# Performance work log

Hardware: AMD Instinct MI355X
Metric: run time of the kernel (lower is better)

The kernel has to match this reference:

```python
import jax, jax.numpy as jnp
import numpy as np

E = 1024      # embed_dim (== embed_dim_)
NH = 8        # num_heads
HD = E // NH  # head_dim
BS1 = 2048
BS2 = 2048
EPS = 1e-5


def _layernorm(x, g, b):
    m = jnp.mean(x, axis=-1, keepdims=True)
    v = jnp.mean(jnp.square(x - m), axis=-1, keepdims=True)
    return (x - m) * jax.lax.rsqrt(v + EPS) * g + b


def setup_inputs() -> dict:
    key = jax.random.key(0)
    ks = jax.random.split(key, 16)
    s = 1.0 / np.sqrt(E)
    s4 = 1.0 / np.sqrt(4 * E)
    inp = {
        "x1": jax.random.normal(ks[0], (BS1, E), jnp.float32),
        "x2": jax.random.normal(ks[1], (BS2, E), jnp.float32),
        "Wq": jax.random.uniform(ks[2], (E, E), jnp.float32, -s, s),
        "bq": jax.random.uniform(ks[3], (E,), jnp.float32, -s, s),
        "Wk": jax.random.uniform(ks[4], (E, E), jnp.float32, -s, s),
        "bk": jax.random.uniform(ks[5], (E,), jnp.float32, -s, s),
        "Wv": jax.random.uniform(ks[6], (E, E), jnp.float32, -s, s),
        "bv": jax.random.uniform(ks[7], (E,), jnp.float32, -s, s),
        "Wo": jax.random.uniform(ks[8], (E, E), jnp.float32, -s, s),
        "bo": jax.random.uniform(ks[9], (E,), jnp.float32, -s, s),
        "W1": jax.random.uniform(ks[10], (4 * E, E), jnp.float32, -s, s),
        "b1": jax.random.uniform(ks[11], (4 * E,), jnp.float32, -s, s),
        "W2": jax.random.uniform(ks[12], (E, 4 * E), jnp.float32, -s4, s4),
        "b2": jax.random.uniform(ks[13], (E,), jnp.float32, -s4, s4),
        "g1": jnp.ones((E,), jnp.float32),
        "be1": jnp.zeros((E,), jnp.float32),
        "g2": jnp.ones((E,), jnp.float32),
        "be2": jnp.zeros((E,), jnp.float32),
    }
    return inp


def reference(x1, x2, Wq, bq, Wk, bk, Wv, bv, Wo, bo, W1, b1, W2, b2, g1, be1, g2, be2):
    scale = HD ** -0.5
    # Projections; attention runs over the batch axis (n=bs1, m=bs2)
    q = (x1 @ Wq.T + bq).reshape(BS1, NH, HD)   # [n,h,d]
    k = (x2 @ Wk.T + bk).reshape(BS2, NH, HD)   # [m,h,d]
    v = (x2 @ Wv.T + bv).reshape(BS2, NH, HD)   # [m,h,d]
    scores = jnp.einsum('nhd,mhd->nmh', q, k) * scale  # [n,m,h]
    # NOTE: faithful to source: softmax over the HEADS axis (dim=-1)
    probs = jax.nn.softmax(scores, axis=-1)
    # dropout is identity in eval mode
    attn = jnp.einsum('nmh,mhd->nhd', probs, v).reshape(BS1, E)
    attn = attn @ Wo.T + bo
    h = _layernorm(x1 + attn, g1, be1)
    ffn = jax.nn.relu(h @ W1.T + b1) @ W2.T + b2
    return _layernorm(h + ffn, g2, be2)
```

## Files before the change

kernel.cpp:

```cpp
#include <hip/hip_runtime.h>

#define BS 2048
#define EMB 1024
#define NHEAD 8
#define HDIM 128

typedef unsigned short u16;
typedef __attribute__((ext_vector_type(8))) short bf16x8;
typedef __attribute__((ext_vector_type(4))) float f32x4;

__device__ __forceinline__ u16 f32_bf16(float f) {
  unsigned u = __float_as_uint(f);
  u += 0x7fffu + ((u >> 16) & 1u);
  return (u16)(u >> 16);
}
__device__ __forceinline__ float bf2f(u16 x) {
  return __uint_as_float((unsigned)x << 16);
}

__device__ __forceinline__ void gld_lds16(const void* g, void* l) {
  __builtin_amdgcn_global_load_lds(
      (const __attribute__((address_space(1))) void*)g,
      (__attribute__((address_space(3))) void*)l, 16, 0, 0);
}

struct CvtArgs { const float* src[8]; };
__global__ __launch_bounds__(256) void cvt_all(CvtArgs a, u16* __restrict__ dst) {
  long i = (long)blockIdx.x * 256 + threadIdx.x;
  int seg = (int)(i >> 18);
  const float* src; long b;
  if (seg < 2)       { src = a.src[0]; b = 0; }
  else if (seg < 4)  { src = a.src[1]; b = 2L << 18; }
  else if (seg == 4) { src = a.src[2]; b = 4L << 18; }
  else if (seg == 5) { src = a.src[3]; b = 5L << 18; }
  else if (seg == 6) { src = a.src[4]; b = 6L << 18; }
  else if (seg == 7) { src = a.src[5]; b = 7L << 18; }
  else if (seg < 12) { src = a.src[6]; b = 8L << 18; }
  else               { src = a.src[7]; b = 12L << 18; }
  float4 v = ((const float4*)src)[i - b];
  ushort4 o;
  o.x = f32_bf16(v.x); o.y = f32_bf16(v.y); o.z = f32_bf16(v.z); o.w = f32_bf16(v.w);
  ((ushort4*)dst)[i] = o;
}

__device__ __forceinline__ void gemm_core(
    const u16* __restrict__ A, const u16* __restrict__ B, void* __restrict__ Cp,
    const float* __restrict__ bias, int K, int lda, int ldb, int ldc,
    long cbase, int mode, int relu, int m0, int n0) {
  __shared__ __align__(16) u16 As[128 * 32];
  __shared__ __align__(16) u16 Bs[128 * 32];
  const int t = threadIdx.x;
  const int lane = t & 63, l15 = lane & 15, quad = lane >> 4;
  const int wv = t >> 6, wr = wv & 1, wc = wv >> 1;
  const int wbase = t & ~63;

  f32x4 acc[4][4];
#pragma unroll
  for (int r = 0; r < 4; ++r)
#pragma unroll
    for (int c = 0; c < 4; ++c) acc[r][c] = (f32x4){0.f, 0.f, 0.f, 0.f};

  for (int k0 = 0; k0 < K; k0 += 32) {
#pragma unroll
    for (int i = 0; i < 2; ++i) {
      int s = i * 256 + t;
      gld_lds16(A + (long)(m0 + (s >> 2)) * lda + k0 + (s & 3) * 8,
                As + (i * 256 + wbase) * 8);
    }
#pragma unroll
    for (int i = 0; i < 2; ++i) {
      int s = i * 256 + t;
      gld_lds16(B + (long)(n0 + (s >> 2)) * ldb + k0 + (s & 3) * 8,
                Bs + (i * 256 + wbase) * 8);
    }
    __syncthreads();
    bf16x8 fa[4], fb[4];
#pragma unroll
    for (int r = 0; r < 4; ++r)
      fa[r] = *(const bf16x8*)&As[(wr * 64 + r * 16 + l15) * 32 + quad * 8];
#pragma unroll
    for (int c = 0; c < 4; ++c)
      fb[c] = *(const bf16x8*)&Bs[(wc * 64 + c * 16 + l15) * 32 + quad * 8];
#pragma unroll
    for (int r = 0; r < 4; ++r)
#pragma unroll
      for (int c = 0; c < 4; ++c)
        acc[r][c] = __builtin_amdgcn_mfma_f32_16x16x32_bf16(fa[r], fb[c], acc[r][c], 0, 0, 0);
    __syncthreads();
  }

#pragma unroll
  for (int r = 0; r < 4; ++r)
#pragma unroll
    for (int c = 0; c < 4; ++c) {
      const int m = m0 + wr * 64 + r * 16 + quad * 4;
      const int n = n0 + wc * 64 + c * 16 + l15;
      const float bv = bias ? bias[n] : 0.f;
      f32x4 v = acc[r][c];
      if (mode == 2) {
        ushort4 o;
        o.x = f32_bf16(v[0] + bv);
        o.y = f32_bf16(v[1] + bv);
        o.z = f32_bf16(v[2] + bv);
        o.w = f32_bf16(v[3] + bv);
        *(ushort4*)((u16*)Cp + cbase + (long)n * ldc + m) = o;
      } else {
#pragma unroll
        for (int i = 0; i < 4; ++i) {
          float x = v[i] + bv;
          if (relu) x = fmaxf(x, 0.f);
          if (mode == 0)
            ((float*)Cp)[cbase + (long)(m + i) * ldc + n] = x;
          else
            ((u16*)Cp)[cbase + (long)(m + i) * ldc + n] = f32_bf16(x);
        }
      }
    }
}

__global__ __launch_bounds__(256) void gemm_bt_k(
    const u16* __restrict__ A, const u16* __restrict__ B, void* __restrict__ C,
    const float* __restrict__ bias, int K, int lda, int ldb, int ldc,
    long aOffZ, long bOffZ, long cOffZ, int mode, int relu) {
  gemm_core(A + (long)blockIdx.z * aOffZ, B + (long)blockIdx.z * bOffZ, C, bias,
            K, lda, ldb, ldc, (long)blockIdx.z * cOffZ, mode, relu,
            blockIdx.y * 128, blockIdx.x * 128);
}

__global__ __launch_bounds__(256) void qkv_kernel(
    const u16* __restrict__ x1b, const u16* __restrict__ x2b,
    const u16* __restrict__ Wqb, const u16* __restrict__ Wkb, const u16* __restrict__ Wvb,
    const float* __restrict__ bq, const float* __restrict__ bk, const float* __restrict__ bv,
    u16* __restrict__ Qb, u16* __restrict__ Kb, u16* __restrict__ Vt) {
  const int z = blockIdx.z;
  const u16* A = (z == 0) ? x1b : x2b;
  const u16* B = (z == 0) ? Wqb : (z == 1) ? Wkb : Wvb;
  void* C = (z == 0) ? (void*)Qb : (z == 1) ? (void*)Kb : (void*)Vt;
  const float* bias = (z == 0) ? bq : (z == 1) ? bk : bv;
  const int mode = (z == 2) ? 2 : 1;
  const int ldc = (z == 2) ? 2048 : 1024;
  gemm_core(A, B, C, bias, 1024, 1024, 1024, ldc, 0, mode, 0,
            blockIdx.y * 128, blockIdx.x * 128);
}

__global__ __launch_bounds__(1024, 4) void attn_fused(
    const u16* __restrict__ Q, const u16* __restrict__ Km, const u16* __restrict__ Vt,
    u16* __restrict__ p0, u16* __restrict__ p1, u16* __restrict__ p2, u16* __restrict__ p3) {
  __shared__ __align__(16) u16 Qs[32 * 1024];
  __shared__ __align__(16) u16 Ps[8 * 32 * 128];
  const int t = threadIdx.x;
  const int lane = t & 63, l15 = lane & 15, quad = lane >> 4;
  const int w = t >> 6, wbase = t & ~63;
  const int mw = w & 7, nh = w >> 3;
  const int n0 = blockIdx.x * 32;
  const int mz = blockIdx.y * 512;
  u16* part = (blockIdx.y == 0) ? p0 : (blockIdx.y == 1) ? p1 : (blockIdx.y == 2) ? p2 : p3;

#pragma unroll
  for (int i = 0; i < 4; ++i) {
    int s = i * 1024 + t;
    int n = s >> 7;
    int kel = (((s & 127) << 3) ^ ((n & 7) << 3));
    gld_lds16(Q + (long)(n0 + n) * 1024 + kel, Qs + (i * 1024 + wbase) * 8);
  }

  const int nq = nh * 16 + l15;
  const int swz3 = (nq & 7) << 3;
  const int swz4 = (nq & 7) << 4;

  f32x4 accp[8];
#pragma unroll
  for (int c = 0; c < 8; ++c) accp[c] = (f32x4){0.f, 0.f, 0.f, 0.f};

  for (int it = 0; it < 4; ++it) {
    __syncthreads();
    f32x4 accs[8];
#pragma unroll
    for (int h = 0; h < 8; ++h) accs[h] = (f32x4){0.f, 0.f, 0.f, 0.f};
    const u16* krow = Km + (long)(mz + it * 128 + mw * 16 + l15) * 1024;
#pragma unroll
    for (int h = 0; h < 8; ++h)
#pragma unroll
      for (int kk = 0; kk < 4; ++kk) {
        bf16x8 kf = *(const bf16x8*)&krow[h * 128 + kk * 32 + quad * 8];
        bf16x8 qf = *(const bf16x8*)&Qs[nq * 1024 + ((h * 128 + kk * 32 + quad * 8) ^ swz3)];
        accs[h] = __builtin_amdgcn_mfma_f32_16x16x32_bf16(kf, qf, accs[h], 0, 0, 0);
      }
    const float scale = 0.08838834764831845f;
#pragma unroll
    for (int i = 0; i < 4; ++i) {
      float mx = accs[0][i];
#pragma unroll
      for (int h = 1; h < 8; ++h) mx = fmaxf(mx, accs[h][i]);
      float sum = 0.f;
#pragma unroll
      for (int h = 0; h < 8; ++h) {
        float e = __expf((accs[h][i] - mx) * scale);
        accs[h][i] = e;
        sum += e;
      }
      float inv = 1.f / sum;
#pragma unroll
      for (int h = 0; h < 8; ++h) accs[h][i] *= inv;
    }
#pragma unroll
    for (int h = 0; h < 8; ++h) {
      ushort4 o;
      o.x = f32_bf16(accs[h][0]);
      o.y = f32_bf16(accs[h][1]);
      o.z = f32_bf16(accs[h][2]);
      o.w = f32_bf16(accs[h][3]);
      *(ushort4*)((char*)Ps + h * 8192 + nq * 256 + ((mw * 32 + quad * 8) ^ swz4)) = o;
    }
    __syncthreads();
#pragma unroll
    for (int mq = 0; mq < 4; ++mq) {
      bf16x8 pa = *(const bf16x8*)((const char*)Ps + mw * 8192 + nq * 256 +
                                   ((mq * 64 + quad * 16) ^ swz4));
      const u16* vb = Vt + (long)(mw * 128) * 2048 + mz + it * 128 + mq * 32 + quad * 8;
#pragma unroll
      for (int c = 0; c < 8; ++c) {
        bf16x8 vf = *(const bf16x8*)&vb[(long)(c * 16 + l15) * 2048];
        accp[c] = __builtin_amdgcn_mfma_f32_16x16x32_bf16(pa, vf, accp[c], 0, 0, 0);
      }
    }
  }
#pragma unroll
  for (int c = 0; c < 8; ++c)
#pragma unroll
    for (int i = 0; i < 4; ++i)
      part[(long)(n0 + nh * 16 + quad * 4 + i) * 1024 + mw * 128 + c * 16 + l15] =
          f32_bf16(accp[c][i]);
}

__global__ __launch_bounds__(256) void reduce4p_bf16(
    const u16* __restrict__ p0, const u16* __restrict__ p1,
    const u16* __restrict__ p2, const u16* __restrict__ p3, u16* __restrict__ out) {
  long i = (long)blockIdx.x * 256 + threadIdx.x;
  ushort4 a = ((const ushort4*)p0)[i];
  ushort4 b = ((const ushort4*)p1)[i];
  ushort4 c = ((const ushort4*)p2)[i];
  ushort4 d = ((const ushort4*)p3)[i];
  ushort4 o;
  o.x = f32_bf16(bf2f(a.x) + bf2f(b.x) + bf2f(c.x) + bf2f(d.x));
  o.y = f32_bf16(bf2f(a.y) + bf2f(b.y) + bf2f(c.y) + bf2f(d.y));
  o.z = f32_bf16(bf2f(a.z) + bf2f(b.z) + bf2f(c.z) + bf2f(d.z));
  o.w = f32_bf16(bf2f(a.w) + bf2f(b.w) + bf2f(c.w) + bf2f(d.w));
  ((ushort4*)out)[i] = o;
}

__global__ __launch_bounds__(256) void ln_residual_p4(
    const float* __restrict__ x,
    const u16* __restrict__ p0, const u16* __restrict__ p1,
    const u16* __restrict__ p2, const u16* __restrict__ p3,
    const float* __restrict__ colb, const float* __restrict__ g, const float* __restrict__ b,
    float* __restrict__ out32, u16* __restrict__ out16) {
  const int row = blockIdx.x, t = threadIdx.x;
  const long base = (long)row * EMB;
  float4 v = ((const float4*)(x + base))[t];
  ushort4 a0 = ((const ushort4*)(p0 + base))[t];
  ushort4 a1 = ((const ushort4*)(p1 + base))[t];
  ushort4 a2 = ((const ushort4*)(p2 + base))[t];
  ushort4 a3 = ((const ushort4*)(p3 + base))[t];
  float4 cb = ((const float4*)colb)[t];
  v.x += bf2f(a0.x) + bf2f(a1.x) + bf2f(a2.x) + bf2f(a3.x) + cb.x;
  v.y += bf2f(a0.y) + bf2f(a1.y) + bf2f(a2.y) + bf2f(a3.y) + cb.y;
  v.z += bf2f(a0.z) + bf2f(a1.z) + bf2f(a2.z) + bf2f(a3.z) + cb.z;
  v.w += bf2f(a0.w) + bf2f(a1.w) + bf2f(a2.w) + bf2f(a3.w) + cb.w;
  float s = v.x + v.y + v.z + v.w;
  float q = v.x * v.x + v.y * v.y + v.z * v.z + v.w * v.w;
#pragma unroll
  for (int off = 32; off > 0; off >>= 1) {
    s += __shfl_xor(s, off);
    q += __shfl_xor(q, off);
  }
  __shared__ float red[8];
  const int wv = t >> 6, lane = t & 63;
  if (lane == 0) { red[wv] = s; red[4 + wv] = q; }
  __syncthreads();
  s = red[0] + red[1] + red[2] + red[3];
  q = red[4] + red[5] + red[6] + red[7];
  const float mean = s * (1.f / EMB);
  const float var = q * (1.f / EMB) - mean * mean;
  const float rstd = rsqrtf(var + 1e-5f);
  float4 gg = ((const float4*)g)[t];
  float4 bb = ((const float4*)b)[t];
  float4 o;
  o.x = (v.x - mean) * rstd * gg.x + bb.x;
  o.y = (v.y - mean) * rstd * gg.y + bb.y;
  o.z = (v.z - mean) * rstd * gg.z + bb.z;
  o.w = (v.w - mean) * rstd * gg.w + bb.w;
  ((float4*)(out32 + base))[t] = o;
  if (out16) {
    ushort4 ho;
    ho.x = f32_bf16(o.x); ho.y = f32_bf16(o.y); ho.z = f32_bf16(o.z); ho.w = f32_bf16(o.w);
    ((ushort4*)(out16 + base))[t] = ho;
  }
}

extern "C" void kernel_launch(void* const* d_in, const int* in_sizes, int n_in,
                              void* d_out, int out_size, void* d_ws, size_t ws_size,
                              hipStream_t stream) {
  const float* x1 = (const float*)d_in[0];
  const float* x2 = (const float*)d_in[1];
  const float* Wq = (const float*)d_in[2];
  const float* bq = (const float*)d_in[3];
  const float* Wk = (const float*)d_in[4];
  const float* bk = (const float*)d_in[5];
  const float* Wv = (const float*)d_in[6];
  const float* bv = (const float*)d_in[7];
  const float* Wo = (const float*)d_in[8];
  const float* bo = (const float*)d_in[9];
  const float* W1 = (const float*)d_in[10];
  const float* b1 = (const float*)d_in[11];
  const float* W2 = (const float*)d_in[12];
  const float* b2 = (const float*)d_in[13];
  const float* g1 = (const float*)d_in[14];
  const float* be1 = (const float*)d_in[15];
  const float* g2 = (const float*)d_in[16];
  const float* be2 = (const float*)d_in[17];

  char* ws = (char*)d_ws;
  const size_t MB = 1ull << 20;
  u16* x1b = (u16*)(ws + 0 * MB);
  u16* x2b = (u16*)(ws + 4 * MB);
  u16* Wqb = (u16*)(ws + 8 * MB);
  u16* Wkb = (u16*)(ws + 10 * MB);
  u16* Wvb = (u16*)(ws + 12 * MB);
  u16* Wob = (u16*)(ws + 14 * MB);
  u16* W1b = (u16*)(ws + 16 * MB);
  u16* W2b = (u16*)(ws + 24 * MB);
  u16* Qb  = (u16*)(ws + 32 * MB);
  u16* Kb  = (u16*)(ws + 36 * MB);
  u16* Vtb = (u16*)(ws + 40 * MB);
  u16* attnb = (u16*)(ws + 44 * MB);
  u16* aP[4] = {(u16*)(ws + 48 * MB), (u16*)(ws + 52 * MB),
                (u16*)(ws + 56 * MB), (u16*)(ws + 60 * MB)};
  u16* woP[4] = {(u16*)(ws + 48 * MB), (u16*)(ws + 52 * MB),
                 (u16*)(ws + 56 * MB), (u16*)(ws + 60 * MB)};
  float* h32  = (float*)(ws + 64 * MB);
  u16*  h16   = (u16*)(ws + 72 * MB);
  u16*  ffn1b = (u16*)(ws + 76 * MB);
  u16* f2P[4] = {(u16*)(ws + 92 * MB), (u16*)(ws + 96 * MB),
                 (u16*)(ws + 100 * MB), (u16*)(ws + 104 * MB)};

  CvtArgs ca;
  ca.src[0] = x1; ca.src[1] = x2; ca.src[2] = Wq; ca.src[3] = Wk;
  ca.src[4] = Wv; ca.src[5] = Wo; ca.src[6] = W1; ca.src[7] = W2;
  cvt_all<<<16384, 256, 0, stream>>>(ca, (u16*)ws);

  qkv_kernel<<<dim3(8, 16, 3), 256, 0, stream>>>(x1b, x2b, Wqb, Wkb, Wvb, bq, bk, bv, Qb, Kb, Vtb);

  attn_fused<<<dim3(64, 4), 1024, 0, stream>>>(Qb, Kb, Vtb, aP[0], aP[1], aP[2], aP[3]);

  reduce4p_bf16<<<2048, 256, 0, stream>>>(aP[0], aP[1], aP[2], aP[3], attnb);

  gemm_bt_k<<<dim3(8, 16, 4), 256, 0, stream>>>(attnb, Wob, woP[0], nullptr,
                                                256, 1024, 1024, 1024,
                                                256, 256, (long)BS * 1024, 1, 0);

  ln_residual_p4<<<2048, 256, 0, stream>>>(x1, woP[0], woP[1], woP[2], woP[3],
                                           bo, g1, be1, h32, h16);

  gemm_bt_k<<<dim3(32, 16, 1), 256, 0, stream>>>(h16, W1b, ffn1b, b1,
                                                 1024, 1024, 1024, 4096,
                                                 0, 0, 0, 1, 1);

  gemm_bt_k<<<dim3(8, 16, 4), 256, 0, stream>>>(ffn1b, W2b, f2P[0], nullptr,
                                                1024, 4096, 4096, 1024,
                                                1024, 1024, (long)BS * 1024, 1, 0);

  ln_residual_p4<<<2048, 256, 0, stream>>>(h32, f2P[0], f2P[1], f2P[2], f2P[3],
                                           b2, g2, be2, (float*)d_out, nullptr);
}
```

Baseline: 389.5 us.

## Shrink attention block to 16 query rows and read Q directly from global

The attention kernel now processes 16 query rows per block with 512 threads, not 32 rows with 1024 threads, and launches twice as many blocks. The Q tile is no longer staged into LDS; each wave loads Q fragments straight from global memory, and K/V fragment loads are batched ahead of the MFMA chains. This removes the large LDS allocation and the initial barrier so more blocks can be resident and loads can overlap. In exchange, K and V are re-read from global/L2 by twice as many blocks.

Measured after the change: 447.1 us. +14.8%, slower.

```diff
diff --git a/kernel.cpp b/kernel.cpp
--- a/kernel.cpp
+++ b/kernel.cpp
@@ -143,49 +143,43 @@
             blockIdx.y * 128, blockIdx.x * 128);
 }
 
-__global__ __launch_bounds__(1024, 4) void attn_fused(
+__global__ __launch_bounds__(512, 4) void attn_fused(
     const u16* __restrict__ Q, const u16* __restrict__ Km, const u16* __restrict__ Vt,
     u16* __restrict__ p0, u16* __restrict__ p1, u16* __restrict__ p2, u16* __restrict__ p3) {
-  __shared__ __align__(16) u16 Qs[32 * 1024];
-  __shared__ __align__(16) u16 Ps[8 * 32 * 128];
+  __shared__ __align__(16) u16 Ps[8 * 16 * 128];
   const int t = threadIdx.x;
   const int lane = t & 63, l15 = lane & 15, quad = lane >> 4;
-  const int w = t >> 6, wbase = t & ~63;
-  const int mw = w & 7, nh = w >> 3;
-  const int n0 = blockIdx.x * 32;
+  const int w = t >> 6;
+  const int n0 = blockIdx.x * 16;
   const int mz = blockIdx.y * 512;
   u16* part = (blockIdx.y == 0) ? p0 : (blockIdx.y == 1) ? p1 : (blockIdx.y == 2) ? p2 : p3;
 
-#pragma unroll
-  for (int i = 0; i < 4; ++i) {
-    int s = i * 1024 + t;
-    int n = s >> 7;
-    int kel = (((s & 127) << 3) ^ ((n & 7) << 3));
-    gld_lds16(Q + (long)(n0 + n) * 1024 + kel, Qs + (i * 1024 + wbase) * 8);
-  }
-
-  const int nq = nh * 16 + l15;
-  const int swz3 = (nq & 7) << 3;
-  const int swz4 = (nq & 7) << 4;
-
   f32x4 accp[8];
 #pragma unroll
   for (int c = 0; c < 8; ++c) accp[c] = (f32x4){0.f, 0.f, 0.f, 0.f};
 
+  const u16* qrow = Q + (long)(n0 + l15) * 1024 + quad * 8;
+
   for (int it = 0; it < 4; ++it) {
-    __syncthreads();
+    const int mb = mz + it * 128;
     f32x4 accs[8];
 #pragma unroll
     for (int h = 0; h < 8; ++h) accs[h] = (f32x4){0.f, 0.f, 0.f, 0.f};
-    const u16* krow = Km + (long)(mz + it * 128 + mw * 16 + l15) * 1024;
-#pragma unroll
-    for (int h = 0; h < 8; ++h)
+
+    const u16* krow = Km + (long)(mb + w * 16 + l15) * 1024 + quad * 8;
+#pragma unroll
+    for (int h = 0; h < 8; ++h) {
+      bf16x8 kf[4], qf[4];
 #pragma unroll
       for (int kk = 0; kk < 4; ++kk) {
-        bf16x8 kf = *(const bf16x8*)&krow[h * 128 + kk * 32 + quad * 8];
-        bf16x8 qf = *(const bf16x8*)&Qs[nq * 1024 + ((h * 128 + kk * 32 + quad * 8) ^ swz3)];
-        accs[h] = __builtin_amdgcn_mfma_f32_16x16x32_bf16(kf, qf, accs[h], 0, 0, 0);
+        kf[kk] = *(const bf16x8*)&krow[h * 128 + kk * 32];
+        qf[kk] = *(const bf16x8*)&qrow[h * 128 + kk * 32];
       }
+#pragma unroll
+      for (int kk = 0; kk < 4; ++kk)
+        accs[h] = __builtin_amdgcn_mfma_f32_16x16x32_bf16(kf[kk], qf[kk], accs[h], 0, 0, 0);
+    }
+
     const float scale = 0.08838834764831845f;
 #pragma unroll
     for (int i = 0; i < 4; ++i) {
@@ -203,6 +197,8 @@
 #pragma unroll
       for (int h = 0; h < 8; ++h) accs[h][i] *= inv;
     }
+
+    __syncthreads();
 #pragma unroll
     for (int h = 0; h < 8; ++h) {
       ushort4 o;
@@ -210,26 +206,29 @@
       o.y = f32_bf16(accs[h][1]);
       o.z = f32_bf16(accs[h][2]);
       o.w = f32_bf16(accs[h][3]);
-      *(ushort4*)((char*)Ps + h * 8192 + nq * 256 + ((mw * 32 + quad * 8) ^ swz4)) = o;
+      *(ushort4*)((char*)Ps + h * 4096 + l15 * 256 +
+                  ((w * 32 + quad * 8) ^ ((l15 & 7) << 4))) = o;
     }
     __syncthreads();
 #pragma unroll
     for (int mq = 0; mq < 4; ++mq) {
-      bf16x8 pa = *(const bf16x8*)((const char*)Ps + mw * 8192 + nq * 256 +
-                                   ((mq * 64 + quad * 16) ^ swz4));
-      const u16* vb = Vt + (long)(mw * 128) * 2048 + mz + it * 128 + mq * 32 + quad * 8;
-#pragma unroll
-      for (int c = 0; c < 8; ++c) {
-        bf16x8 vf = *(const bf16x8*)&vb[(long)(c * 16 + l15) * 2048];
-        accp[c] = __builtin_amdgcn_mfma_f32_16x16x32_bf16(pa, vf, accp[c], 0, 0, 0);
-      }
+      bf16x8 vf[8];
+#pragma unroll
+      for (int c = 0; c < 8; ++c)
+        vf[c] = *(const bf16x8*)&Vt[(long)(w * 128 + c * 16 + l15) * 2048 +
+                                    mb + mq * 32 + quad * 8];
+      bf16x8 pa = *(const bf16x8*)((const char*)Ps + w * 4096 + l15 * 256 +
+                                   ((mq * 64 + quad * 16) ^ ((l15 & 7) << 4)));
+#pragma unroll
+      for (int c = 0; c < 8; ++c)
+        accp[c] = __builtin_amdgcn_mfma_f32_16x16x32_bf16(pa, vf[c], accp[c], 0, 0, 0);
     }
   }
 #pragma unroll
   for (int c = 0; c < 8; ++c)
 #pragma unroll
     for (int i = 0; i < 4; ++i)
-      part[(long)(n0 + nh * 16 + quad * 4 + i) * 1024 + mw * 128 + c * 16 + l15] =
+      part[(long)(n0 + quad * 4 + i) * 1024 + w * 128 + c * 16 + l15] =
           f32_bf16(accp[c][i]);
 }
 
@@ -351,7 +350,7 @@
 
   qkv_kernel<<<dim3(8, 16, 3), 256, 0, stream>>>(x1b, x2b, Wqb, Wkb, Wvb, bq, bk, bv, Qb, Kb, Vtb);
 
-  attn_fused<<<dim3(64, 4), 1024, 0, stream>>>(Qb, Kb, Vtb, aP[0], aP[1], aP[2], aP[3]);
+  attn_fused<<<dim3(128, 4), 512, 0, stream>>>(Qb, Kb, Vtb, aP[0], aP[1], aP[2], aP[3]);
 
   reduce4p_bf16<<<2048, 256, 0, stream>>>(aP[0], aP[1], aP[2], aP[3], attnb);
 
```
